# Kernel tuning notes

Measured on AMD Instinct MI355X. Metric: run time of the kernel, lower is better.

## Reference

```python
import jax, jax.numpy as jnp
import numpy as np

B, S, D = 4, 2048, 1024
NUM_CODES = 16384


def setup_inputs() -> dict:
    key = jax.random.key(0)
    k1, k2 = jax.random.split(key)
    inputs = jax.random.normal(k1, (B, S, D), dtype=jnp.float32)
    codebook = jax.random.normal(k2, (NUM_CODES, D), dtype=jnp.float32)
    return {"inputs": inputs, "codebook": codebook, "kcodes": 8}


def reference(inputs, codebook, kcodes):
    # logits = -cdist(inputs, codebook, p=2); squared distance is monotonic
    # with euclidean distance, so top-k indices are identical (no sqrt needed).
    x2 = jnp.sum(inputs * inputs, axis=-1, keepdims=True)        # [B,S,1]
    c2 = jnp.sum(codebook * codebook, axis=-1)                   # [C]
    xc = jnp.einsum('bsd,cd->bsc', inputs, codebook)             # [B,S,C]
    logits = -(x2 - 2.0 * xc + c2)                               # -squared dist
    _, codebook_ids = jax.lax.top_k(logits, kcodes)              # [B,S,K]
    gathered = codebook[codebook_ids]                            # [B,S,K,D]
    outputs = gathered.sum(axis=-2) / kcodes                     # [B,S,D]
    return outputs, codebook_ids
```

## Files before the change

### kernel.cpp

```cpp
#include <hip/hip_runtime.h>
#include <hip/hip_bf16.h>
#include <float.h>

#define R_TOTAL 8192
#define D_DIM   1024
#define C_TOTAL 16384
#define KSEL    8
#define XN  ((size_t)R_TOTAL * D_DIM)
#define CBN ((size_t)C_TOTAL * D_DIM)
#define NSPLIT  8
#define SEGC    (C_TOTAL / NSPLIT)
#define NCHUNK  (SEGC / 256)
#define NKT     (NCHUNK * 16)
#define NC_RES  24

typedef __attribute__((ext_vector_type(8)))  short short8v;
typedef __attribute__((ext_vector_type(16))) float f32x16;
typedef __attribute__((ext_vector_type(8)))  unsigned short ushort8;

__device__ __forceinline__ unsigned short f2bf(float f) {
  unsigned u = __float_as_uint(f);
  u = (u + 0x7fffu + ((u >> 16) & 1u)) >> 16;
  return (unsigned short)u;
}

__device__ __forceinline__ void gload_lds16(const void* g, void* l) {
  __builtin_amdgcn_global_load_lds((const __attribute__((address_space(1))) void*)g,
                                   (__attribute__((address_space(3))) void*)l, 16, 0, 0);
}

__global__ void cvt_kernel(const float* __restrict__ X, const float* __restrict__ CB,
                           unsigned short* __restrict__ Xb, unsigned short* __restrict__ CBb) {
  size_t e = ((size_t)blockIdx.x * 256 + threadIdx.x) * 8;
  const float* src; unsigned short* dst; size_t off;
  if (e < XN) { src = X;  dst = Xb;  off = e; }
  else        { src = CB; dst = CBb; off = e - XN; }
  float4 v0 = *(const float4*)(src + off);
  float4 v1 = *(const float4*)(src + off + 4);
  ushort8 o;
  o[0]=f2bf(v0.x); o[1]=f2bf(v0.y); o[2]=f2bf(v0.z); o[3]=f2bf(v0.w);
  o[4]=f2bf(v1.x); o[5]=f2bf(v1.y); o[6]=f2bf(v1.z); o[7]=f2bf(v1.w);
  *(ushort8*)(dst + off) = o;
}

__global__ void c2_kernel(const float* __restrict__ cb, float* __restrict__ c2) {
  const int wave = threadIdx.x >> 6;
  const int lane = threadIdx.x & 63;
  const int code = blockIdx.x * 4 + wave;
  const float* row = cb + (size_t)code * D_DIM;
  float s = 0.f;
  #pragma unroll
  for (int i = 0; i < D_DIM / 64; ++i) { float v = row[lane + i * 64]; s += v * v; }
  #pragma unroll
  for (int off = 32; off >= 1; off >>= 1) s += __shfl_xor(s, off, 64);
  if (lane == 0) c2[code] = s;
}

__global__ __launch_bounds__(512, 2)
void gemm_topk_kernel(const unsigned short* __restrict__ Xb,
                      const unsigned short* __restrict__ CBb,
                      const float* __restrict__ c2g,
                      float* __restrict__ pval, int* __restrict__ pid) {
  extern __shared__ char smem[];
  float* c2s = (float*)(smem + 131072);

  const int t   = threadIdx.x;
  const int wid = t >> 6, l = t & 63;
  const int wr  = wid >> 2;
  const int wc  = wid & 3;
  const int l31 = l & 31, hi = l >> 5;

  const int xt    = blockIdx.x & 31;
  const int seg   = blockIdx.x >> 5;
  const int xbase = xt * 256;
  const int cb0   = seg * SEGC;

  *(float4*)&c2s[t * 4] = *(const float4*)(c2g + cb0 + t * 4);
  asm volatile("s_waitcnt lgkmcnt(0)" ::: "memory");

  const int srow = t >> 3;
  const int sswz = (((t & 7) * 16) ^ ((srow & 7) << 4)) >> 1;
  const int fswz = (l & 7) << 4;

  f32x16 acc[4][2];
  float tv[2][KSEL]; int ti[2][KSEL];
  #pragma unroll
  for (int fm = 0; fm < 4; ++fm)
    #pragma unroll
    for (int fn = 0; fn < 2; ++fn)
      #pragma unroll
      for (int r = 0; r < 16; ++r) acc[fm][fn][r] = 0.f;
  #pragma unroll
  for (int fn = 0; fn < 2; ++fn)
    #pragma unroll
    for (int q = 0; q < KSEL; ++q) { tv[fn][q] = -FLT_MAX; ti[fn][q] = 0; }

  auto STAGE = [&](int g) {
    const int kbase = (g & 15) * 64;
    const int arow0 = cb0 + (g >> 4) * 256;
    char* As = smem + (g & 1) * 32768;
    char* Xs = smem + 65536 + (g & 1) * 32768;
    #pragma unroll
    for (int i = 0; i < 4; ++i)
      gload_lds16(CBb + (size_t)(arow0 + i * 64 + srow) * D_DIM + kbase + sswz,
                  As + (i * 512 + t) * 16);
    #pragma unroll
    for (int i = 0; i < 4; ++i)
      gload_lds16(Xb + (size_t)(xbase + i * 64 + srow) * D_DIM + kbase + sswz,
                  Xs + (i * 512 + t) * 16);
  };

  STAGE(0);

  for (int g = 0; g < NKT; ++g) {
    if (g + 1 < NKT) {
      STAGE(g + 1);
      asm volatile("s_waitcnt vmcnt(8)" ::: "memory");
    } else {
      asm volatile("s_waitcnt vmcnt(0)" ::: "memory");
    }
    __builtin_amdgcn_s_barrier();

    const char* As = smem + (g & 1) * 32768;
    const char* Xs = smem + 65536 + (g & 1) * 32768;

    #pragma unroll
    for (int ks2 = 0; ks2 < 4; ks2 += 2) {
      short8v av[4][2], bv[2][2];
      #pragma unroll
      for (int fm = 0; fm < 4; ++fm)
        #pragma unroll
        for (int j = 0; j < 2; ++j) {
          const int row = wr * 128 + fm * 32 + l31;
          const int kb  = (((ks2 + j) * 32 + hi * 16)) ^ fswz;
          av[fm][j] = *(const short8v*)(As + row * 128 + kb);
        }
      #pragma unroll
      for (int fn = 0; fn < 2; ++fn)
        #pragma unroll
        for (int j = 0; j < 2; ++j) {
          const int row = wc * 64 + fn * 32 + l31;
          const int kb  = (((ks2 + j) * 32 + hi * 16)) ^ fswz;
          bv[fn][j] = *(const short8v*)(Xs + row * 128 + kb);
        }
      __builtin_amdgcn_s_setprio(1);
      #pragma unroll
      for (int fm = 0; fm < 4; ++fm)
        #pragma unroll
        for (int fn = 0; fn < 2; ++fn)
          #pragma unroll
          for (int j = 0; j < 2; ++j)
            acc[fm][fn] = __builtin_amdgcn_mfma_f32_32x32x16_bf16(
                av[fm][j], bv[fn][j], acc[fm][fn], 0, 0, 0);
      __builtin_amdgcn_s_setprio(0);
    }
    __builtin_amdgcn_s_barrier();

    if ((g & 15) == 15) {
      const int ch = g >> 4;
      #pragma unroll
      for (int fm = 0; fm < 4; ++fm) {
        const int rloc = ch * 256 + wr * 128 + fm * 32 + hi * 4;
        const int idb  = cb0 + wr * 128 + ch * 256 + fm * 32 + hi * 4;
        #pragma unroll
        for (int q = 0; q < 4; ++q) {
          const float4 cq = *(const float4*)&c2s[rloc + q * 8];
          #pragma unroll
          for (int fn = 0; fn < 2; ++fn) {
            #pragma unroll
            for (int r = 0; r < 4; ++r) {
              const float c2v = (r == 0) ? cq.x : (r == 1) ? cq.y : (r == 2) ? cq.z : cq.w;
              const float s = 2.f * acc[fm][fn][q * 4 + r] - c2v;
              if (s > tv[fn][KSEL - 1]) {
                float cv = s; int ci = idb + q * 8 + r;
                #pragma unroll
                for (int q2 = 0; q2 < KSEL; ++q2) {
                  if (cv > tv[fn][q2]) {
                    const float t0 = tv[fn][q2]; tv[fn][q2] = cv; cv = t0;
                    const int   t1 = ti[fn][q2]; ti[fn][q2] = ci; ci = t1;
                  }
                }
              }
            }
          }
        }
      }
      #pragma unroll
      for (int fm = 0; fm < 4; ++fm)
        #pragma unroll
        for (int fn = 0; fn < 2; ++fn)
          #pragma unroll
          for (int r = 0; r < 16; ++r) acc[fm][fn][r] = 0.f;
    }
  }

  asm volatile("s_waitcnt vmcnt(0)" ::: "memory");
  __builtin_amdgcn_s_barrier();
  float* mv = (float*)smem;
  int*   mi = (int*)(smem + 32768);
  #pragma unroll
  for (int fn = 0; fn < 2; ++fn) {
    const int xrL = wc * 64 + fn * 32 + l31;
    const int li  = wr * 2 + hi;
    #pragma unroll
    for (int q = 0; q < KSEL; ++q) {
      mv[xrL * 32 + li * 8 + q] = tv[fn][q];
      mi[xrL * 32 + li * 8 + q] = ti[fn][q];
    }
  }
  __syncthreads();
  if (t < 256) {
    float bvv[KSEL]; int bii[KSEL];
    #pragma unroll
    for (int q = 0; q < KSEL; ++q) { bvv[q] = -FLT_MAX; bii[q] = 0x7fffffff; }
    for (int c = 0; c < 32; ++c) {
      float cv = mv[t * 32 + c]; int ci = mi[t * 32 + c];
      if (cv > bvv[KSEL - 1] || (cv == bvv[KSEL - 1] && ci < bii[KSEL - 1])) {
        #pragma unroll
        for (int q = 0; q < KSEL; ++q) {
          if (cv > bvv[q] || (cv == bvv[q] && ci < bii[q])) {
            const float t0 = bvv[q]; bvv[q] = cv; cv = t0;
            const int   t1 = bii[q]; bii[q] = ci; ci = t1;
          }
        }
      }
    }
    const size_t base = ((size_t)(xbase + t) * NSPLIT + seg) * KSEL;
    #pragma unroll
    for (int q = 0; q < KSEL; ++q) { pval[base + q] = bvv[q]; pid[base + q] = bii[q]; }
  }
}

__global__ __launch_bounds__(256)
void rescore_kernel(const float* __restrict__ X, const float* __restrict__ CB,
                    const float* __restrict__ c2g,
                    const float* __restrict__ pval, const int* __restrict__ pid,
                    float* __restrict__ out, float* __restrict__ out_ids, int nsplit) {
  const int row = blockIdx.x;
  const int t = threadIdx.x;
  __shared__ float xs[D_DIM];
  __shared__ int   scid[NC_RES];
  __shared__ float sv[NC_RES];
  __shared__ int   topid[KSEL];

  *(float4*)&xs[t * 4] = *(const float4*)(X + (size_t)row * D_DIM + t * 4);

  const int ncand = nsplit * KSEL;
  const int NC = NC_RES < ncand ? NC_RES : ncand;

  if (t < 64) {
    float v = -FLT_MAX; int idv = 0x7fffffff;
    if (t < ncand) {
      v   = pval[(size_t)row * ncand + t];
      idv = pid[(size_t)row * ncand + t];
    }
    for (int it = 0; it < NC; ++it) {
      float bv = v; int bid = idv;
      #pragma unroll
      for (int off = 32; off >= 1; off >>= 1) {
        float ov = __shfl_xor(bv, off, 64);
        int   oi = __shfl_xor(bid, off, 64);
        if (ov > bv || (ov == bv && oi < bid)) { bv = ov; bid = oi; }
      }
      if (t == 0) scid[it] = bid;
      if (idv == bid) v = -FLT_MAX;
    }
  }
  __syncthreads();

  const int w = t >> 6, ln = t & 63;
  for (int c = w; c < NC; c += 4) {
    const int id = scid[c];
    const float* cr = CB + (size_t)id * D_DIM;
    float s = 0.f;
    #pragma unroll
    for (int i = 0; i < 4; ++i) {
      const float4 cv = *(const float4*)(cr + ln * 4 + i * 256);
      const float4 xv = *(const float4*)&xs[ln * 4 + i * 256];
      s += cv.x * xv.x + cv.y * xv.y + cv.z * xv.z + cv.w * xv.w;
    }
    #pragma unroll
    for (int off = 32; off >= 1; off >>= 1) s += __shfl_xor(s, off, 64);
    if (ln == 0) sv[c] = 2.f * s - c2g[id];
  }
  __syncthreads();

  if (t == 0) {
    float bv[KSEL]; int bi[KSEL];
    #pragma unroll
    for (int q = 0; q < KSEL; ++q) { bv[q] = -FLT_MAX; bi[q] = 0x7fffffff; }
    for (int c = 0; c < NC; ++c) {
      float cv = sv[c]; int ci = scid[c];
      #pragma unroll
      for (int q = 0; q < KSEL; ++q) {
        if (cv > bv[q] || (cv == bv[q] && ci < bi[q])) {
          const float t0 = bv[q]; bv[q] = cv; cv = t0;
          const int   t1 = bi[q]; bi[q] = ci; ci = t1;
        }
      }
    }
    #pragma unroll
    for (int q = 0; q < KSEL; ++q) {
      topid[q] = bi[q];
      out_ids[(size_t)row * KSEL + q] = (float)bi[q];
    }
  }
  __syncthreads();

  float4 a = {0.f, 0.f, 0.f, 0.f};
  #pragma unroll
  for (int q = 0; q < KSEL; ++q) {
    const float4 cv = *(const float4*)(CB + (size_t)topid[q] * D_DIM + t * 4);
    a.x += cv.x; a.y += cv.y; a.z += cv.z; a.w += cv.w;
  }
  a.x *= 0.125f; a.y *= 0.125f; a.z *= 0.125f; a.w *= 0.125f;
  *(float4*)(out + (size_t)row * D_DIM + t * 4) = a;
}

extern "C" void kernel_launch(void* const* d_in, const int* in_sizes, int n_in,
                              void* d_out, int out_size, void* d_ws, size_t ws_size,
                              hipStream_t stream) {
  const float* X  = (const float*)d_in[0];
  const float* CB = (const float*)d_in[1];

  float* out     = (float*)d_out;
  float* out_ids = out + XN;

  const size_t XbB  = XN * 2;
  const size_t CBbB = CBN * 2;
  const size_t c2B  = C_TOTAL * 4;
  const size_t pvB  = (size_t)R_TOTAL * NSPLIT * KSEL * 4;

  char* p = (char*)d_ws;
  unsigned short* Xb;
  unsigned short* CBb;
  if (ws_size >= XbB + CBbB + c2B + 2 * pvB) {
    Xb  = (unsigned short*)p; p += XbB;
    CBb = (unsigned short*)p; p += CBbB;
  } else {
    CBb = (unsigned short*)d_out;
    Xb  = (unsigned short*)p; p += XbB;
  }
  float* c2   = (float*)p; p += c2B;
  float* pval = (float*)p; p += pvB;
  int*   pid  = (int*)p;

  hipLaunchKernelGGL(cvt_kernel, dim3((unsigned)((XN + CBN) / 8 / 256)), dim3(256), 0, stream,
                     X, CB, Xb, CBb);
  hipLaunchKernelGGL(c2_kernel, dim3(C_TOTAL / 4), dim3(256), 0, stream, CB, c2);
  hipLaunchKernelGGL(gemm_topk_kernel, dim3(32 * NSPLIT), dim3(512), 136 * 1024, stream,
                     Xb, CBb, c2, pval, pid);
  hipLaunchKernelGGL(rescore_kernel, dim3(R_TOTAL), dim3(256), 0, stream,
                     X, CB, c2, pval, pid, out, out_ids, NSPLIT);
}
```

Measured before the change: 602.1 us.

## Interleave next-tile prefetch with MFMA sub-phases in GEMM top-k loop

Splits tile staging into separate codebook and input loads and issues them inside the first two of four k sub-phases. Each sub-phase now reads its own fragments, runs its MFMAs and synchronises with barriers, with a single vmcnt wait before the next tile. The goal is to spread global-to-LDS traffic across the compute instead of issuing it all at the top of the tile. In exchange, barriers per tile rise from two to eight, and the latency hiding now depends on how the loads fall between sub-phases.

```diff
diff --git a/kernel.cpp b/kernel.cpp
--- a/kernel.cpp
+++ b/kernel.cpp
@@ -76,7 +76,6 @@
   const int cb0   = seg * SEGC;
 
   *(float4*)&c2s[t * 4] = *(const float4*)(c2g + cb0 + t * 4);
-  asm volatile("s_waitcnt lgkmcnt(0)" ::: "memory");
 
   const int srow = t >> 3;
   const int sswz = (((t & 7) * 16) ^ ((srow & 7) << 4)) >> 1;
@@ -95,73 +94,68 @@
     #pragma unroll
     for (int q = 0; q < KSEL; ++q) { tv[fn][q] = -FLT_MAX; ti[fn][q] = 0; }
 
-  auto STAGE = [&](int g) {
+  auto STAGE_A = [&](int g) {
     const int kbase = (g & 15) * 64;
     const int arow0 = cb0 + (g >> 4) * 256;
     char* As = smem + (g & 1) * 32768;
-    char* Xs = smem + 65536 + (g & 1) * 32768;
     #pragma unroll
     for (int i = 0; i < 4; ++i)
       gload_lds16(CBb + (size_t)(arow0 + i * 64 + srow) * D_DIM + kbase + sswz,
                   As + (i * 512 + t) * 16);
+  };
+  auto STAGE_X = [&](int g) {
+    const int kbase = (g & 15) * 64;
+    char* Xs = smem + 65536 + (g & 1) * 32768;
     #pragma unroll
     for (int i = 0; i < 4; ++i)
       gload_lds16(Xb + (size_t)(xbase + i * 64 + srow) * D_DIM + kbase + sswz,
                   Xs + (i * 512 + t) * 16);
   };
 
-  STAGE(0);
+  STAGE_A(0); STAGE_X(0);
+  asm volatile("s_waitcnt vmcnt(0) lgkmcnt(0)" ::: "memory");
+  __builtin_amdgcn_s_barrier();
 
   for (int g = 0; g < NKT; ++g) {
-    if (g + 1 < NKT) {
-      STAGE(g + 1);
-      asm volatile("s_waitcnt vmcnt(8)" ::: "memory");
-    } else {
-      asm volatile("s_waitcnt vmcnt(0)" ::: "memory");
-    }
-    __builtin_amdgcn_s_barrier();
-
     const char* As = smem + (g & 1) * 32768;
     const char* Xs = smem + 65536 + (g & 1) * 32768;
 
     #pragma unroll
-    for (int ks2 = 0; ks2 < 4; ks2 += 2) {
-      short8v av[4][2], bv[2][2];
+    for (int p = 0; p < 4; ++p) {
+      short8v av[4], bv[2];
+      const int kb = (p * 32 + hi * 16) ^ fswz;
       #pragma unroll
       for (int fm = 0; fm < 4; ++fm)
-        #pragma unroll
-        for (int j = 0; j < 2; ++j) {
-          const int row = wr * 128 + fm * 32 + l31;
-          const int kb  = (((ks2 + j) * 32 + hi * 16)) ^ fswz;
-          av[fm][j] = *(const short8v*)(As + row * 128 + kb);
-        }
+        av[fm] = *(const short8v*)(As + (wr * 128 + fm * 32 + l31) * 128 + kb);
       #pragma unroll
       for (int fn = 0; fn < 2; ++fn)
-        #pragma unroll
-        for (int j = 0; j < 2; ++j) {
-          const int row = wc * 64 + fn * 32 + l31;
-          const int kb  = (((ks2 + j) * 32 + hi * 16)) ^ fswz;
-          bv[fn][j] = *(const short8v*)(Xs + row * 128 + kb);
-        }
+        bv[fn] = *(const short8v*)(Xs + (wc * 64 + fn * 32 + l31) * 128 + kb);
+
+      if (p == 0 && g + 1 < NKT) STAGE_A(g + 1);
+      if (p == 1 && g + 1 < NKT) STAGE_X(g + 1);
+
+      __builtin_amdgcn_s_barrier();
+
       __builtin_amdgcn_s_setprio(1);
       #pragma unroll
       for (int fm = 0; fm < 4; ++fm)
         #pragma unroll
         for (int fn = 0; fn < 2; ++fn)
-          #pragma unroll
-          for (int j = 0; j < 2; ++j)
-            acc[fm][fn] = __builtin_amdgcn_mfma_f32_32x32x16_bf16(
-                av[fm][j], bv[fn][j], acc[fm][fn], 0, 0, 0);
+          acc[fm][fn] = __builtin_amdgcn_mfma_f32_32x32x16_bf16(
+              av[fm], bv[fn], acc[fm][fn], 0, 0, 0);
       __builtin_amdgcn_s_setprio(0);
-    }
-    __builtin_amdgcn_s_barrier();
+
+      if (p == 3)
+        asm volatile("s_waitcnt vmcnt(0)" ::: "memory");
+      __builtin_amdgcn_s_barrier();
+    }
 
     if ((g & 15) == 15) {
       const int ch = g >> 4;
       #pragma unroll
       for (int fm = 0; fm < 4; ++fm) {
         const int rloc = ch * 256 + wr * 128 + fm * 32 + hi * 4;
-        const int idb  = cb0 + wr * 128 + ch * 256 + fm * 32 + hi * 4;
+        const int idb  = cb0 + ch * 256 + wr * 128 + fm * 32 + hi * 4;
         #pragma unroll
         for (int q = 0; q < 4; ++q) {
           const float4 cq = *(const float4*)&c2s[rloc + q * 8];
@@ -194,7 +188,7 @@
     }
   }
 
-  asm volatile("s_waitcnt vmcnt(0)" ::: "memory");
+  asm volatile("s_waitcnt vmcnt(0) lgkmcnt(0)" ::: "memory");
   __builtin_amdgcn_s_barrier();
   float* mv = (float*)smem;
   int*   mi = (int*)(smem + 32768);
```

After: 610.6 us. About the same (+1.4%).
